# Kernel optimization log

Hardware: AMD Instinct MI355X
Metric: run time of the kernel (lower is better)

The kernel has to match this reference:

```python
import jax, jax.numpy as jnp
import numpy as np

# config
L, N, D, H, I = 4, 16, 64, 1024, 4096   # layers, heads, head_dim, hidden, intermediate
V, P = 50257, 8192                       # vocab, positions
B, S = 2, 2048                           # batch, seq
EPS = 1e-5


def setup_inputs() -> dict:
    key = jax.random.key(0)
    ks = jax.random.split(key, 20)
    std = 0.02
    inp = {
        "input_ids": jax.random.randint(ks[0], (B, S), 0, V),
        "position_ids": jnp.broadcast_to(jnp.arange(S), (B, S)),
        "wte": jax.random.normal(ks[1], (V, H), jnp.float32) * std,
        "wpe": jax.random.normal(ks[2], (P, H), jnp.float32) * std,
        # per-layer stacked params; torch Linear weights are (out, in)
        "ln1_w": jnp.ones((L, H), jnp.float32),
        "ln1_b": jnp.zeros((L, H), jnp.float32),
        "cattn_w": jax.random.normal(ks[3], (L, H + 2 * D, H), jnp.float32) * std,
        "cattn_b": jnp.zeros((L, H + 2 * D), jnp.float32),
        "cproj_w": jax.random.normal(ks[4], (L, H, H), jnp.float32) * std,
        "cproj_b": jnp.zeros((L, H), jnp.float32),
        "ln2_w": jnp.ones((L, H), jnp.float32),
        "ln2_b": jnp.zeros((L, H), jnp.float32),
        "fc_w": jax.random.normal(ks[5], (L, I, H), jnp.float32) * std,
        "fc_b": jnp.zeros((L, I), jnp.float32),
        "mproj_w": jax.random.normal(ks[6], (L, H, I), jnp.float32) * std,
        "mproj_b": jnp.zeros((L, H), jnp.float32),
        "lnf_w": jnp.ones((H,), jnp.float32),
        "lnf_b": jnp.zeros((H,), jnp.float32),
    }
    return inp


def _ln(x, w, b):
    mu = jnp.mean(x, axis=-1, keepdims=True)
    var = jnp.mean(jnp.square(x - mu), axis=-1, keepdims=True)
    return (x - mu) * jax.lax.rsqrt(var + EPS) * w + b


def _forward(input_ids, position_ids, wte, wpe, ln1_w, ln1_b, cattn_w, cattn_b,
             cproj_w, cproj_b, ln2_w, ln2_b, fc_w, fc_b, mproj_w, mproj_b,
             lnf_w, lnf_b):
    h = wte[input_ids] + wpe[position_ids]              # [B,S,H]
    b, s, _ = h.shape
    causal = jnp.tril(jnp.ones((s, s), bool))[None, :, None, :]   # [1,S,1,S] keep-mask
    neg = jnp.finfo(jnp.float32).min
    for l in range(L):
        # --- attention ---
        resid = h
        x = _ln(h, ln1_w[l], ln1_b[l])
        qkv = x @ cattn_w[l].T + cattn_b[l]             # [B,S,H+2D]
        q = qkv[..., :H].reshape(b, s, N, D)
        k = qkv[..., H:H + D]                           # [B,S,D] shared key head
        v = qkv[..., H + D:]                            # [B,S,D] shared value head
        unscale = float(l + 1)
        scale = 1.0 / (unscale * np.sqrt(D))
        scores = jnp.einsum('bsnd,btd->bsnt', q, k) * scale
        # upcast_masked_softmax: to fp32, re-multiply by unscale, mask, softmax
        scores = scores.astype(jnp.float32) * unscale
        scores = jnp.where(causal, scores, neg)
        attn = jax.nn.softmax(scores, axis=-1).astype(h.dtype)
        out = jnp.einsum('bsnt,btd->bsnd', attn, v).reshape(b, s, H)
        h = resid + (out @ cproj_w[l].T + cproj_b[l])
        # --- mlp ---
        resid = h
        x = _ln(h, ln2_w[l], ln2_b[l])
        x = jax.nn.gelu(x @ fc_w[l].T + fc_b[l], approximate=False)
        h = resid + (x @ mproj_w[l].T + mproj_b[l])
    return _ln(h, lnf_w, lnf_b)


def reference(input_ids, position_ids, wte, wpe, ln1_w, ln1_b, cattn_w, cattn_b,
              cproj_w, cproj_b, ln2_w, ln2_b, fc_w, fc_b, mproj_w, mproj_b,
              lnf_w, lnf_b):
    return _forward(input_ids, position_ids, wte, wpe, ln1_w, ln1_b, cattn_w,
                    cattn_b, cproj_w, cproj_b, ln2_w, ln2_b, fc_w, fc_b,
                    mproj_w, mproj_b, lnf_w, lnf_b)
```

## Files before the change

### kernel.cpp

```cpp
#include <hip/hip_runtime.h>
#include <math.h>

typedef __attribute__((ext_vector_type(8))) short short8;
typedef __attribute__((ext_vector_type(8))) __bf16 bf16x8;
typedef __attribute__((ext_vector_type(4))) float f32x4;

static constexpr int H = 1024, LNUM = 4, SEQ = 2048, BATCH = 2;
static constexpr int TOK = BATCH * SEQ;
static constexpr int NI = 4096, QKVD = H + 128;

__device__ __forceinline__ short f2bf(float f) {
  union { float f; unsigned u; } c; c.f = f;
  return (short)((c.u + 0x7fffu + ((c.u >> 16) & 1u)) >> 16);
}

__device__ __forceinline__ void gl_lds16(const short* g, short* l) {
  __builtin_amdgcn_global_load_lds(
      (const __attribute__((address_space(1))) unsigned*)g,
      (__attribute__((address_space(3))) unsigned*)l, 16, 0, 0);
}

__device__ __forceinline__ unsigned cvtpk_bf16(float lo, float hi) {
  unsigned r;
  asm("v_cvt_pk_bf16_f32 %0, %1, %2" : "=v"(r) : "v"(lo), "v"(hi));
  return r;
}

#define MFMA16(a, b, c) __builtin_amdgcn_mfma_f32_16x16x32_bf16(a, b, c, 0, 0, 0)

__global__ __launch_bounds__(256) void embed_kernel(
    const int* __restrict__ ids, const int* __restrict__ pos,
    const float* __restrict__ wte, const float* __restrict__ wpe,
    float* __restrict__ h) {
  int i = blockIdx.x * 256 + threadIdx.x;
  int tok = i >> 10, d = i & 1023;
  h[i] = wte[(size_t)ids[tok] * H + d] + wpe[(size_t)pos[tok] * H + d];
}

__global__ __launch_bounds__(256) void cast_kernel(
    const float* __restrict__ src, short* __restrict__ dst) {
  int i = blockIdx.x * 256 + threadIdx.x;
  float4 v = ((const float4*)src)[i];
  union { short s[4]; uint2 u; } p;
  p.s[0] = f2bf(v.x); p.s[1] = f2bf(v.y); p.s[2] = f2bf(v.z); p.s[3] = f2bf(v.w);
  ((uint2*)dst)[i] = p.u;
}

template <bool BF16_OUT>
__global__ __launch_bounds__(256) void ln_kernel(
    const float* __restrict__ X, const float* __restrict__ w,
    const float* __restrict__ b, void* __restrict__ out) {
  int row = blockIdx.x;
  const float* x = X + (size_t)row * H;
  int tid = threadIdx.x, lane = tid & 63, wid = tid >> 6;
  float v[4];
#pragma unroll
  for (int i = 0; i < 4; i++) v[i] = x[tid + i * 256];
  float s = v[0] + v[1] + v[2] + v[3];
#pragma unroll
  for (int off = 32; off > 0; off >>= 1) s += __shfl_xor(s, off);
  __shared__ float red[8];
  if (lane == 0) red[wid] = s;
  __syncthreads();
  float mu = (red[0] + red[1] + red[2] + red[3]) * (1.0f / H);
  float q = 0.f;
#pragma unroll
  for (int i = 0; i < 4; i++) { float d = v[i] - mu; q += d * d; }
#pragma unroll
  for (int off = 32; off > 0; off >>= 1) q += __shfl_xor(q, off);
  if (lane == 0) red[4 + wid] = q;
  __syncthreads();
  float var = (red[4] + red[5] + red[6] + red[7]) * (1.0f / H);
  float inv = rsqrtf(var + 1e-5f);
#pragma unroll
  for (int i = 0; i < 4; i++) {
    int col = tid + i * 256;
    float r = (v[i] - mu) * inv * w[col] + b[col];
    if (BF16_OUT) ((short*)out)[(size_t)row * H + col] = f2bf(r);
    else          ((float*)out)[(size_t)row * H + col] = r;
  }
}

template <int MODE>
__global__ __launch_bounds__(256) void gemm_mfma(
    const short* __restrict__ A, const short* __restrict__ W,
    const float* __restrict__ bias, void* __restrict__ Cv,
    int M, int N, int K) {
  __shared__ short As[128 * 32];
  __shared__ short Bs[128 * 32];
  int tid = threadIdx.x, wave = tid >> 6, lane = tid & 63;
  int li = lane & 15, lg = lane >> 4;
  int row0 = blockIdx.y * 128, col0 = blockIdx.x * 128;
  int wm = (wave & 1) * 64, wn = (wave >> 1) * 64;
  f32x4 acc[4][4] = {};
  const short* Ab = A + (size_t)(row0 + (tid >> 2)) * K + (tid & 3) * 8;
  const short* Wb = W + (size_t)(col0 + (tid >> 2)) * K + (tid & 3) * 8;
  for (int k0 = 0; k0 < K; k0 += 32) {
    __syncthreads();
    gl_lds16(Ab + k0,            As + tid * 8);
    gl_lds16(Ab + k0 + 64 * K,   As + 2048 + tid * 8);
    gl_lds16(Wb + k0,            Bs + tid * 8);
    gl_lds16(Wb + k0 + 64 * K,   Bs + 2048 + tid * 8);
    __syncthreads();
    bf16x8 af[4], bfr[4];
#pragma unroll
    for (int i = 0; i < 4; ++i) {
      af[i]  = *(const bf16x8*)&As[(wm + i * 16 + li) * 32 + lg * 8];
      bfr[i] = *(const bf16x8*)&Bs[(wn + i * 16 + li) * 32 + lg * 8];
    }
#pragma unroll
    for (int i = 0; i < 4; ++i)
#pragma unroll
      for (int j = 0; j < 4; ++j) acc[i][j] = MFMA16(af[i], bfr[j], acc[i][j]);
  }
  float* Cf = (float*)Cv;
  short* Cs = (short*)Cv;
#pragma unroll
  for (int i = 0; i < 4; ++i) {
    int gr = row0 + wm + i * 16 + lg * 4;
#pragma unroll
    for (int j = 0; j < 4; ++j) {
      int gc = col0 + wn + j * 16 + li;
      float bv = bias[gc];
#pragma unroll
      for (int r = 0; r < 4; ++r) {
        float v = acc[i][j][r] + bv;
        size_t idx = (size_t)(gr + r) * N + gc;
        if (MODE == 1) {
          Cf[idx] += v;
        } else if (MODE == 2) {
          v = 0.5f * v * (1.0f + erff(v * 0.70710678118654752f));
          Cs[idx] = f2bf(v);
        } else {
          Cs[idx] = f2bf(v);
        }
      }
    }
  }
}

__global__ __launch_bounds__(256) void vtrans_kernel(
    const short* __restrict__ qkv, short* __restrict__ vt) {
  int i = blockIdx.x * 256 + threadIdx.x;
  int d  = i & 63;
  int tc = (i >> 6) & 255;
  int b  = i >> 14;
  const short* src = qkv + ((size_t)(b * SEQ + tc * 8)) * QKVD + 1088 + d;
  short8 v;
#pragma unroll
  for (int e = 0; e < 8; ++e) v[e] = src[(size_t)e * QKVD];
  *(short8*)(vt + ((size_t)(b * 64 + d)) * SEQ + tc * 8) = v;
}

__global__ __launch_bounds__(256) void mqa_attn(
    const short* __restrict__ qkv, const short* __restrict__ vtg,
    short* __restrict__ out) {
  int head = blockIdx.y, b = blockIdx.z;
  int s = (blockIdx.x + head * 8) & 31;
  int qt = (s & 1) ? (31 - (s >> 1)) : (s >> 1);
  int tid = threadIdx.x, wave = tid >> 6, lane = tid & 63;
  int li = lane & 15, lg = lane >> 4;

  __shared__ short Kc[64 * 72];
  __shared__ short Vt[64 * 72];

  const size_t qrow0 = (size_t)(b * SEQ + qt * 64);
  bf16x8 qf[2];
  {
    const short* qp = qkv + (qrow0 + wave * 16 + li) * QKVD + head * 64 + lg * 8;
    qf[0] = *(const bf16x8*)(qp);
    qf[1] = *(const bf16x8*)(qp + 32);
  }
  f32x4 oacc[4] = {};
  float m_i = -1e30f, l_i = 0.f;

  int t_ = tid >> 3, c_ = tid & 7;
  const short* kg = qkv + (size_t)(b * SEQ) * QKVD + 1024;
  const short* vg = vtg + (size_t)(b * 64 + t_) * SEQ;

  for (int j = 0; j <= qt; ++j) {
    __syncthreads();
    {
      const short* g0 = kg + (size_t)(j * 64 + t_) * QKVD + c_ * 8;
      short8 k0 = *(const short8*)(g0);
      short8 k1 = *(const short8*)(g0 + 32 * QKVD);
      short8 v0 = *(const short8*)(vg + j * 64 + c_ * 8);
      short8 v1 = *(const short8*)(vg + 32 * SEQ + j * 64 + c_ * 8);
      *(short8*)&Kc[t_ * 72 + c_ * 8] = k0;
      *(short8*)&Kc[(t_ + 32) * 72 + c_ * 8] = k1;
      *(short8*)&Vt[t_ * 72 + c_ * 8] = v0;
      *(short8*)&Vt[(t_ + 32) * 72 + c_ * 8] = v1;
    }
    __syncthreads();

    f32x4 s4[4];
#pragma unroll
    for (int n = 0; n < 4; ++n) {
      bf16x8 kf0 = *(const bf16x8*)&Kc[(n * 16 + li) * 72 + lg * 8];
      bf16x8 kf1 = *(const bf16x8*)&Kc[(n * 16 + li) * 72 + 32 + lg * 8];
      f32x4 a = {};
      a = MFMA16(kf0, qf[0], a);
      a = MFMA16(kf1, qf[1], a);
      s4[n] = a;
    }
    bool diag = (j == qt);
    float p[4][4];
#pragma unroll
    for (int n = 0; n < 4; ++n)
#pragma unroll
      for (int r = 0; r < 4; ++r) {
        float v = s4[n][r] * 0.125f;
        if (diag && (n * 16 + lg * 4 + r) > (wave * 16 + li)) v = -1e30f;
        p[n][r] = v;
      }
    float mx = p[0][0];
#pragma unroll
    for (int n = 0; n < 4; ++n)
#pragma unroll
      for (int r = 0; r < 4; ++r) mx = fmaxf(mx, p[n][r]);
    mx = fmaxf(mx, __shfl_xor(mx, 16));
    mx = fmaxf(mx, __shfl_xor(mx, 32));
    float mn = fmaxf(m_i, mx);
    float alpha = __expf(m_i - mn);
    m_i = mn;
    float ps = 0.f;
#pragma unroll
    for (int n = 0; n < 4; ++n)
#pragma unroll
      for (int r = 0; r < 4; ++r) { float e = __expf(p[n][r] - mn); p[n][r] = e; ps += e; }
    ps += __shfl_xor(ps, 16);
    ps += __shfl_xor(ps, 32);
    l_i = l_i * alpha + ps;
    float arow[4];
#pragma unroll
    for (int r = 0; r < 4; ++r) arow[r] = __shfl(alpha, (lane >> 4) * 20 + r);
#pragma unroll
    for (int dn = 0; dn < 4; ++dn)
#pragma unroll
      for (int r = 0; r < 4; ++r) oacc[dn][r] *= arow[r];
    unsigned pk[4][2];
#pragma unroll
    for (int n = 0; n < 4; ++n) {
      pk[n][0] = cvtpk_bf16(p[n][0], p[n][1]);
      pk[n][1] = cvtpk_bf16(p[n][2], p[n][3]);
    }
#pragma unroll
    for (int ks = 0; ks < 2; ++ks) {
      union { unsigned w[4]; bf16x8 v; } pu;
#pragma unroll
      for (int d = 0; d < 4; ++d) {
        int sl = (li + ((lg & 1) << 5) + ((d >> 1) << 4)) << 2;
        unsigned a0 = __builtin_amdgcn_ds_bpermute(sl, (int)pk[2 * ks][d & 1]);
        unsigned a1 = __builtin_amdgcn_ds_bpermute(sl, (int)pk[2 * ks + 1][d & 1]);
        pu.w[d] = (lg >> 1) ? a1 : a0;
      }
#pragma unroll
      for (int dn = 0; dn < 4; ++dn) {
        bf16x8 vf = *(const bf16x8*)&Vt[(dn * 16 + li) * 72 + ks * 32 + lg * 8];
        oacc[dn] = MFMA16(pu.v, vf, oacc[dn]);
      }
    }
  }
  float lrow[4];
#pragma unroll
  for (int r = 0; r < 4; ++r) lrow[r] = __shfl(l_i, (lane >> 4) * 20 + r);
#pragma unroll
  for (int r = 0; r < 4; ++r) {
    float inv = 1.0f / lrow[r];
    size_t row = (qrow0 + wave * 16 + lg * 4 + r) * H + head * 64;
#pragma unroll
    for (int dn = 0; dn < 4; ++dn) out[row + dn * 16 + li] = f2bf(oacc[dn][r] * inv);
  }
}

extern "C" void kernel_launch(void* const* d_in, const int* in_sizes, int n_in,
                              void* d_out, int out_size, void* d_ws, size_t ws_size,
                              hipStream_t stream) {
  const int*   input_ids    = (const int*)d_in[0];
  const int*   position_ids = (const int*)d_in[1];
  const float* wte     = (const float*)d_in[2];
  const float* wpe     = (const float*)d_in[3];
  const float* ln1_w   = (const float*)d_in[4];
  const float* ln1_b   = (const float*)d_in[5];
  const float* cattn_w = (const float*)d_in[6];
  const float* cattn_b = (const float*)d_in[7];
  const float* cproj_w = (const float*)d_in[8];
  const float* cproj_b = (const float*)d_in[9];
  const float* ln2_w   = (const float*)d_in[10];
  const float* ln2_b   = (const float*)d_in[11];
  const float* fc_w    = (const float*)d_in[12];
  const float* fc_b    = (const float*)d_in[13];
  const float* mproj_w = (const float*)d_in[14];
  const float* mproj_b = (const float*)d_in[15];
  const float* lnf_w   = (const float*)d_in[16];
  const float* lnf_b   = (const float*)d_in[17];

  float* h     = (float*)d_ws;
  short* xbf   = (short*)(h + (size_t)TOK * H);
  short* qkvbf = xbf + (size_t)TOK * H;
  short* fcbf  = qkvbf + (size_t)TOK * QKVD;
  short* wqkv  = fcbf + (size_t)TOK * NI;
  short* wcp   = wqkv + (size_t)QKVD * H;
  short* wfc   = wcp + (size_t)H * H;
  short* wmp   = wfc + (size_t)NI * H;
  short* vtg   = fcbf;

  embed_kernel<<<TOK * H / 256, 256, 0, stream>>>(input_ids, position_ids, wte, wpe, h);

  for (int l = 0; l < LNUM; l++) {
    cast_kernel<<<QKVD * H / 1024, 256, 0, stream>>>(cattn_w + (size_t)l * QKVD * H, wqkv);
    cast_kernel<<<H * H / 1024, 256, 0, stream>>>(cproj_w + (size_t)l * H * H, wcp);
    cast_kernel<<<NI * H / 1024, 256, 0, stream>>>(fc_w + (size_t)l * NI * H, wfc);
    cast_kernel<<<H * NI / 1024, 256, 0, stream>>>(mproj_w + (size_t)l * H * NI, wmp);

    ln_kernel<true><<<TOK, 256, 0, stream>>>(h, ln1_w + l * H, ln1_b + l * H, xbf);
    gemm_mfma<0><<<dim3(QKVD / 128, TOK / 128), 256, 0, stream>>>(
        xbf, wqkv, cattn_b + (size_t)l * QKVD, qkvbf, TOK, QKVD, H);
    vtrans_kernel<<<(2 * 64 * SEQ / 8) / 256, 256, 0, stream>>>(qkvbf, vtg);
    mqa_attn<<<dim3(32, 16, BATCH), 256, 0, stream>>>(qkvbf, vtg, xbf);
    gemm_mfma<1><<<dim3(H / 128, TOK / 128), 256, 0, stream>>>(
        xbf, wcp, cproj_b + (size_t)l * H, h, TOK, H, H);
    ln_kernel<true><<<TOK, 256, 0, stream>>>(h, ln2_w + l * H, ln2_b + l * H, xbf);
    gemm_mfma<2><<<dim3(NI / 128, TOK / 128), 256, 0, stream>>>(
        xbf, wfc, fc_b + (size_t)l * NI, fcbf, TOK, NI, H);
    gemm_mfma<1><<<dim3(H / 128, TOK / 128), 256, 0, stream>>>(
        fcbf, wmp, mproj_b + (size_t)l * H, h, TOK, H, NI);
  }
  ln_kernel<false><<<TOK, 256, 0, stream>>>(h, lnf_w, lnf_b, d_out);
}
```

Baseline: 1.834 ms.

## Add 256x256-tile 512-thread GEMM with split-K atomics for MLP layers

Adds a new GEMM kernel with 256x256 output tiles, 512 threads, double-buffered direct global-to-LDS loads with XOR swizzle, and a grouped block-ID swizzle for L2 locality. It is used for the fc GEMM (with fused GELU) and for the mproj GEMM. The mproj GEMM is split four ways along K and accumulated into the residual with atomicAdd, with bias added only by the first split. The larger tiles are meant to raise data reuse and MFMA density. The costs are fewer blocks for fc (256) and heavy fp32 atomic traffic, which also makes the summation order nondeterministic.

```diff
diff --git a/kernel.cpp b/kernel.cpp
--- a/kernel.cpp
+++ b/kernel.cpp
@@ -139,6 +139,102 @@
   }
 }
 
+template <int MODE>
+__global__ __launch_bounds__(512) void gemm256(
+    const short* __restrict__ A, const short* __restrict__ W,
+    const float* __restrict__ bias, void* __restrict__ Cv,
+    int N, int K) {
+  __shared__ short lds[2][2][256 * 64];
+  int tid = threadIdx.x, wave = tid >> 6, lane = tid & 63;
+  int li = lane & 15, lg = lane >> 4;
+  int gx = gridDim.x;
+  int id = blockIdx.y * gx + blockIdx.x;
+  int cpx = (gx * gridDim.y) >> 3;
+  int swz = (id & 7) * cpx + (id >> 3);
+  int bx = swz % gx, by = swz / gx;
+  int row0 = by * 256, col0 = bx * 256;
+  const short* Ab = A + (size_t)row0 * K + (blockIdx.z << 10);
+  const short* Wb = W + (size_t)col0 * K + (blockIdx.z << 10);
+  int wrow = (wave & 1) << 7, wcol = (wave >> 1) << 6;
+  f32x4 acc[8][4] = {};
+
+  auto STAGE = [&](int t, int buf) {
+#pragma unroll
+    for (int i = 0; i < 4; ++i) {
+      int c = i * 512 + tid, r = c >> 3, g = (c & 7) ^ (r & 7);
+      gl_lds16(Ab + (size_t)r * K + t * 64 + g * 8, &lds[buf][0][c * 8]);
+      gl_lds16(Wb + (size_t)r * K + t * 64 + g * 8, &lds[buf][1][c * 8]);
+    }
+  };
+  STAGE(0, 0);
+  STAGE(1, 1);
+  for (int t = 0; t < 16; ++t) {
+    int cur = t & 1;
+    if (t < 15) { asm volatile("s_waitcnt vmcnt(8)" ::: "memory"); }
+    else        { asm volatile("s_waitcnt vmcnt(0)" ::: "memory"); }
+    __builtin_amdgcn_s_barrier();
+    asm volatile("" ::: "memory");
+    const short* Al = lds[cur][0];
+    const short* Bl = lds[cur][1];
+    bf16x8 bfr[4][2];
+#pragma unroll
+    for (int j = 0; j < 4; ++j)
+#pragma unroll
+      for (int ks = 0; ks < 2; ++ks) {
+        int rb = wcol + j * 16 + li;
+        int sl = (ks * 4 + lg) ^ (rb & 7);
+        bfr[j][ks] = *(const bf16x8*)&Bl[rb * 64 + sl * 8];
+      }
+#pragma unroll
+    for (int q = 0; q < 4; ++q) {
+      bf16x8 afr[2][2];
+#pragma unroll
+      for (int m2 = 0; m2 < 2; ++m2)
+#pragma unroll
+        for (int ks = 0; ks < 2; ++ks) {
+          int ra = wrow + (q * 2 + m2) * 16 + li;
+          int sl = (ks * 4 + lg) ^ (ra & 7);
+          afr[m2][ks] = *(const bf16x8*)&Al[ra * 64 + sl * 8];
+        }
+      __builtin_amdgcn_s_setprio(1);
+#pragma unroll
+      for (int m2 = 0; m2 < 2; ++m2)
+#pragma unroll
+        for (int j = 0; j < 4; ++j)
+#pragma unroll
+          for (int ks = 0; ks < 2; ++ks)
+            acc[q * 2 + m2][j] = MFMA16(afr[m2][ks], bfr[j][ks], acc[q * 2 + m2][j]);
+      __builtin_amdgcn_s_setprio(0);
+    }
+    asm volatile("" ::: "memory");
+    __builtin_amdgcn_s_barrier();
+    if (t + 2 < 16) STAGE(t + 2, cur);
+  }
+  float* Cf = (float*)Cv;
+  short* Cs = (short*)Cv;
+  bool addb = (blockIdx.z == 0);
+#pragma unroll
+  for (int i = 0; i < 8; ++i) {
+    int gr = row0 + wrow + i * 16 + lg * 4;
+#pragma unroll
+    for (int j = 0; j < 4; ++j) {
+      int gc = col0 + wcol + j * 16 + li;
+      float bv = addb ? bias[gc] : 0.f;
+#pragma unroll
+      for (int r = 0; r < 4; ++r) {
+        float v = acc[i][j][r] + bv;
+        size_t idx = (size_t)(gr + r) * N + gc;
+        if (MODE == 1) {
+          atomicAdd(&Cf[idx], v);
+        } else {
+          v = 0.5f * v * (1.0f + erff(v * 0.70710678118654752f));
+          Cs[idx] = f2bf(v);
+        }
+      }
+    }
+  }
+}
+
 __global__ __launch_bounds__(256) void vtrans_kernel(
     const short* __restrict__ qkv, short* __restrict__ vt) {
   int i = blockIdx.x * 256 + threadIdx.x;
@@ -321,10 +417,10 @@
     gemm_mfma<1><<<dim3(H / 128, TOK / 128), 256, 0, stream>>>(
         xbf, wcp, cproj_b + (size_t)l * H, h, TOK, H, H);
     ln_kernel<true><<<TOK, 256, 0, stream>>>(h, ln2_w + l * H, ln2_b + l * H, xbf);
-    gemm_mfma<2><<<dim3(NI / 128, TOK / 128), 256, 0, stream>>>(
-        xbf, wfc, fc_b + (size_t)l * NI, fcbf, TOK, NI, H);
-    gemm_mfma<1><<<dim3(H / 128, TOK / 128), 256, 0, stream>>>(
-        fcbf, wmp, mproj_b + (size_t)l * H, h, TOK, H, NI);
+    gemm256<2><<<dim3(16, 16, 1), 512, 0, stream>>>(
+        xbf, wfc, fc_b + (size_t)l * NI, fcbf, NI, H);
+    gemm256<1><<<dim3(4, 16, 4), 512, 0, stream>>>(
+        fcbf, wmp, mproj_b + (size_t)l * H, h, H, NI);
   }
   ln_kernel<false><<<TOK, 256, 0, stream>>>(h, lnf_w, lnf_b, d_out);
 }
```

After: 1.675 ms. 8.7% less time.
